# Kernel tuning notes

Measured on AMD Instinct MI355X. Metric: run time of the kernel, lower is better.

## Reference

```python
import jax, jax.numpy as jnp
import numpy as np

N, E = 50000, 1600000
IN_F, EDGE_F, HEADS, OUT_F = 64, 16, 4, 32
NEG_SLOPE = 0.2


def setup_inputs() -> dict:
    key = jax.random.key(0)
    ks = jax.random.split(key, 12)
    s = 0.05
    return {
        "x": jax.random.normal(ks[0], (N, IN_F), jnp.float32),
        "edge_index": jax.random.randint(ks[1], (2, E), 0, N, jnp.int32),
        "edge_attr": jax.random.normal(ks[2], (E, EDGE_F), jnp.float32),
        "W_lin": jax.random.normal(ks[3], (HEADS * OUT_F, IN_F), jnp.float32) * s,
        "w_s": jax.random.normal(ks[4], (OUT_F,), jnp.float32) * s,
        "b_s": jax.random.normal(ks[5], (), jnp.float32) * s,
        "w_t": jax.random.normal(ks[6], (OUT_F,), jnp.float32) * s,
        "b_t": jax.random.normal(ks[7], (), jnp.float32) * s,
        "W_edge": jax.random.normal(ks[8], (HEADS * OUT_F, EDGE_F), jnp.float32) * s,
        "w_e": jax.random.normal(ks[9], (OUT_F,), jnp.float32) * s,
        "b_e": jax.random.normal(ks[10], (), jnp.float32) * s,
        "W_res": jax.random.normal(ks[11], (HEADS * OUT_F, IN_F), jnp.float32) * s,
        "bias": jnp.zeros((HEADS * OUT_F,), jnp.float32),
    }


def reference(x, edge_index, edge_attr, W_lin, w_s, b_s, w_t, b_t, W_edge, w_e, b_e, W_res, bias):
    n = x.shape[0]
    src, dst = edge_index[0], edge_index[1]  # j = source, i = target

    # node projection: [N, H, F]
    xp = (x @ W_lin.T).reshape(n, HEADS, OUT_F)
    # attn_s/attn_t are Linear(F,1) then sum(-1) -> per-node per-head scalar
    a_s = xp @ w_s + b_s  # [N, H]
    a_t = xp @ w_t + b_t  # [N, H]

    # edge feature projection and attention term
    ep = (edge_attr @ W_edge.T).reshape(-1, HEADS, OUT_F)  # [E, H, F]
    a_e = ep @ w_e + b_e  # [E, H]

    # per-edge logits: alpha_j + alpha_i + alpha_edge, leaky_relu
    alpha = a_s[src] + a_t[dst] + a_e  # [E, H]
    alpha = jnp.where(alpha >= 0, alpha, NEG_SLOPE * alpha)

    # segment softmax over edges grouped by target node
    amax = jax.ops.segment_max(alpha, dst, num_segments=n)  # [N, H]
    expv = jnp.exp(alpha - amax[dst])  # [E, H]
    denom = jax.ops.segment_sum(expv, dst, num_segments=n)  # [N, H]
    attn = expv / denom[dst]  # [E, H]

    # weighted messages from source nodes, scatter-add to targets
    msg = attn[..., None] * xp[src]  # [E, H, F]
    out = jax.ops.segment_sum(msg, dst, num_segments=n)  # [N, H, F]
    out = out.reshape(n, HEADS * OUT_F)  # concat heads

    out = out + x @ W_res.T + bias
    return out
```

## Files before the change

kernel.cpp:

```cpp
#include <hip/hip_runtime.h>
#include <hip/hip_fp16.h>
#include <math.h>

#define HEADS 4
#define OUT_F 32
#define HF 128
#define IN_F 64
#define EDGE_F 16

typedef int   v4i __attribute__((ext_vector_type(4)));
typedef float v4f __attribute__((ext_vector_type(4)));
typedef float v2f __attribute__((ext_vector_type(2)));
typedef _Float16 v8h __attribute__((ext_vector_type(8)));


__global__ __launch_bounds__(256) void k_project_mfma(
    const float* __restrict__ x, const float* __restrict__ W_lin,
    const float* __restrict__ W_res, const float* __restrict__ bias,
    const float* __restrict__ w_s, const float* __restrict__ w_t,
    const float* __restrict__ b_s, const float* __restrict__ b_t,
    __half* __restrict__ xp, float* __restrict__ a_s, float* __restrict__ a_t,
    float* __restrict__ out, int* __restrict__ head, int N_, int PB) {
  if (blockIdx.x >= PB) {
    int i = (blockIdx.x - PB) * 256 + threadIdx.x;
    if (i < N_ * 4) head[i] = -1;
    return;
  }
  __shared__ __half sw[256][72];
  __shared__ __half sxh[64][72];
  int t = threadIdx.x;
  {
    const float* wsrc = (t < 128) ? (W_lin + t * IN_F) : (W_res + (size_t)(t - 128) * IN_F);
    const float4* w4 = (const float4*)wsrc;
#pragma unroll
    for (int k8 = 0; k8 < 8; k8++) {
      float4 f0 = w4[k8 * 2 + 0];
      float4 f1 = w4[k8 * 2 + 1];
      *(__half2*)(&sw[t][k8 * 8 + 0]) = __floats2half2_rn(f0.x, f0.y);
      *(__half2*)(&sw[t][k8 * 8 + 2]) = __floats2half2_rn(f0.z, f0.w);
      *(__half2*)(&sw[t][k8 * 8 + 4]) = __floats2half2_rn(f1.x, f1.y);
      *(__half2*)(&sw[t][k8 * 8 + 6]) = __floats2half2_rn(f1.z, f1.w);
    }
  }
  int n0 = blockIdx.x * 64;
  {
    int node = t >> 2, q = t & 3;
    int nn = n0 + node;
    const float4* xs = (const float4*)(x + (size_t)nn * IN_F) + q * 4;
#pragma unroll
    for (int j = 0; j < 4; j++) {
      float4 f = (nn < N_) ? xs[j] : make_float4(0.f, 0.f, 0.f, 0.f);
      int col = q * 16 + j * 4;
      *(__half2*)(&sxh[node][col + 0]) = __floats2half2_rn(f.x, f.y);
      *(__half2*)(&sxh[node][col + 2]) = __floats2half2_rn(f.z, f.w);
    }
  }
  __syncthreads();

  int w = t >> 6, l = t & 63;
  int lm = l & 15, lg = l >> 4;
  int mbase = n0 + w * 16;
  v8h a0 = *(const v8h*)(&sxh[w * 16 + lm][lg * 8]);
  v8h a1 = *(const v8h*)(&sxh[w * 16 + lm][32 + lg * 8]);

  float ws_lo = w_s[lm], ws_hi = w_s[16 + lm];
  float wt_lo = w_t[lm], wt_hi = w_t[16 + lm];
  float bsv = b_s[0], btv = b_t[0];

  float sacc[4] = {0.f, 0.f, 0.f, 0.f};
  float tacc[4] = {0.f, 0.f, 0.f, 0.f};

#pragma unroll
  for (int nt = 0; nt < 16; nt++) {
    v8h b0 = *(const v8h*)(&sw[nt * 16 + lm][lg * 8]);
    v8h b1 = *(const v8h*)(&sw[nt * 16 + lm][32 + lg * 8]);
    v4f d = {0.f, 0.f, 0.f, 0.f};
    d = __builtin_amdgcn_mfma_f32_16x16x32_f16(a0, b0, d, 0, 0, 0);
    d = __builtin_amdgcn_mfma_f32_16x16x32_f16(a1, b1, d, 0, 0, 0);
    if (nt < 8) {
      int c = nt * 16 + lm;
      float wssel = (nt & 1) ? ws_hi : ws_lo;
      float wtsel = (nt & 1) ? wt_hi : wt_lo;
#pragma unroll
      for (int reg = 0; reg < 4; reg++) {
        int m = mbase + lg * 4 + reg;
        if (m < N_) xp[(size_t)m * HF + c] = __float2half(d[reg]);
        sacc[reg] += d[reg] * wssel;
        tacc[reg] += d[reg] * wtsel;
      }
      if (nt & 1) {
        int h = nt >> 1;
#pragma unroll
        for (int reg = 0; reg < 4; reg++) {
#pragma unroll
          for (int dlt = 8; dlt > 0; dlt >>= 1) {
            sacc[reg] += __shfl_xor(sacc[reg], dlt, 64);
            tacc[reg] += __shfl_xor(tacc[reg], dlt, 64);
          }
        }
        if (lm == 0) {
#pragma unroll
          for (int reg = 0; reg < 4; reg++) {
            int m = mbase + lg * 4 + reg;
            if (m < N_) {
              a_s[m * 4 + h] = sacc[reg] + bsv;
              a_t[m * 4 + h] = tacc[reg] + btv;
            }
          }
        }
#pragma unroll
        for (int reg = 0; reg < 4; reg++) { sacc[reg] = 0.f; tacc[reg] = 0.f; }
      }
    } else {
      int c = (nt - 8) * 16 + lm;
      float bv = bias[c];
#pragma unroll
      for (int reg = 0; reg < 4; reg++) {
        int m = mbase + lg * 4 + reg;
        if (m < N_) out[(size_t)m * HF + c] = d[reg] + bv;
      }
    }
  }
}

__global__ __launch_bounds__(256) void k_edge_logits(
    const int* __restrict__ ei, const float* __restrict__ ea,
    const float* __restrict__ W_edge, const float* __restrict__ w_e,
    const float* __restrict__ b_e,
    const float* __restrict__ a_s, const float* __restrict__ a_t,
    int* __restrict__ head, v4i* __restrict__ pay, int E_) {
  __shared__ float sv[64];
  {
    int t = threadIdx.x;
    if (t < 64) {
      int h = t >> 4, cc = t & 15;
      float se = 0.f;
#pragma unroll
      for (int f = 0; f < 32; f++) se += W_edge[(h * 32 + f) * 16 + cc] * w_e[f];
      sv[t] = se;
    }
  }
  __syncthreads();
  int e = blockIdx.x * 256 + threadIdx.x;
  if (e >= E_) return;
  int src = ei[e], dst = ei[E_ + e];
  int nx = atomicExch(head + dst * 4 + (e & 3), e);
  float bev = b_e[0];
  const v4f* ea4 = (const v4f*)(ea + (size_t)e * EDGE_F);
  v4f e0 = __builtin_nontemporal_load(ea4 + 0);
  v4f e1 = __builtin_nontemporal_load(ea4 + 1);
  v4f e2 = __builtin_nontemporal_load(ea4 + 2);
  v4f e3 = __builtin_nontemporal_load(ea4 + 3);
  float4 as4 = *(const float4*)(a_s + src * 4);
  float4 at4 = *(const float4*)(a_t + dst * 4);
  float asv[4] = {as4.x, as4.y, as4.z, as4.w};
  float atv[4] = {at4.x, at4.y, at4.z, at4.w};
  float res[4];
#pragma unroll
  for (int h = 0; h < 4; h++) {
    const float* v = sv + h * 16;
    float ae =
        e0.x * v[0]  + e0.y * v[1]  + e0.z * v[2]  + e0.w * v[3]
      + e1.x * v[4]  + e1.y * v[5]  + e1.z * v[6]  + e1.w * v[7]
      + e2.x * v[8]  + e2.y * v[9]  + e2.z * v[10] + e2.w * v[11]
      + e3.x * v[12] + e3.y * v[13] + e3.z * v[14] + e3.w * v[15];
    float al = asv[h] + atv[h] + ae + bev;
    al = al >= 0.f ? al : 0.2f * al;
    res[h] = __expf(al);
  }
  __half2 h01 = __floats2half2_rn(res[0], res[1]);
  __half2 h23 = __floats2half2_rn(res[2], res[3]);
  v4i pk;
  pk.x = src;
  pk.y = *(int*)&h01;
  pk.z = *(int*)&h23;
  pk.w = nx;
  pay[e] = pk;
}

__global__ __launch_bounds__(256) void k_gather(
    const int* __restrict__ head, const v4i* __restrict__ pay,
    const __half* __restrict__ xp, float* __restrict__ out, int N_, int E_) {
  int wid = threadIdx.x >> 6, lane = threadIdx.x & 63;
  int n = blockIdx.x * 4 + wid;
  if (n >= N_) return;
  int e0 = head[n * 4 + 0], e1 = head[n * 4 + 1];
  int e2 = head[n * 4 + 2], e3 = head[n * 4 + 3];
  if ((e0 & e1 & e2 & e3) < 0 && e0 < 0 && e1 < 0 && e2 < 0 && e3 < 0)
    return;
  int h = lane >> 4;
  float2 acc = make_float2(0.f, 0.f);
  float se = 0.f;
#define EXTRACT_EV(P, EV)                                                \
  {                                                                      \
    unsigned hw = (h < 2) ? (unsigned)(P).y : (unsigned)(P).z;           \
    unsigned bits = (h & 1) ? (hw >> 16) : (hw & 0xffffu);               \
    EV = __half2float(__ushort_as_half((unsigned short)bits));           \
  }
#define ROW_FMA(P, EV)                                                   \
  {                                                                      \
    const __half2* xr = (const __half2*)(xp + (size_t)(P).x * HF);       \
    float2 xv = __half22float2(xr[lane]);                                \
    acc.x += (EV) * xv.x;                                                \
    acc.y += (EV) * xv.y;                                                \
    se += (EV);                                                          \
  }
  while ((e0 | e1 | e2 | e3) >= 0) {
    v4i p0 = pay[e0];
    v4i p1 = pay[e1];
    v4i p2 = pay[e2];
    v4i p3 = pay[e3];
    float ev0, ev1, ev2, ev3;
    EXTRACT_EV(p0, ev0);
    EXTRACT_EV(p1, ev1);
    EXTRACT_EV(p2, ev2);
    EXTRACT_EV(p3, ev3);
    ROW_FMA(p0, ev0);
    ROW_FMA(p1, ev1);
    ROW_FMA(p2, ev2);
    ROW_FMA(p3, ev3);
    e0 = p0.w;
    e1 = p1.w;
    e2 = p2.w;
    e3 = p3.w;
  }
  for (int it = 0; it < E_; ++it) {
    if (e0 < 0 && e1 < 0 && e2 < 0 && e3 < 0) break;
    int s0 = e0 < 0 ? 0 : e0, s1 = e1 < 0 ? 0 : e1;
    int s2 = e2 < 0 ? 0 : e2, s3 = e3 < 0 ? 0 : e3;
    v4i p0 = pay[s0];
    v4i p1 = pay[s1];
    v4i p2 = pay[s2];
    v4i p3 = pay[s3];
    float m0 = e0 < 0 ? 0.f : 1.f, m1 = e1 < 0 ? 0.f : 1.f;
    float m2 = e2 < 0 ? 0.f : 1.f, m3 = e3 < 0 ? 0.f : 1.f;
    float ev0, ev1, ev2, ev3;
    EXTRACT_EV(p0, ev0);
    EXTRACT_EV(p1, ev1);
    EXTRACT_EV(p2, ev2);
    EXTRACT_EV(p3, ev3);
    ev0 *= m0; ev1 *= m1; ev2 *= m2; ev3 *= m3;
    ROW_FMA(p0, ev0);
    ROW_FMA(p1, ev1);
    ROW_FMA(p2, ev2);
    ROW_FMA(p3, ev3);
    e0 = e0 < 0 ? e0 : p0.w;
    e1 = e1 < 0 ? e1 : p1.w;
    e2 = e2 < 0 ? e2 : p2.w;
    e3 = e3 < 0 ? e3 : p3.w;
  }
#undef EXTRACT_EV
#undef ROW_FMA
  float r = 1.f / se;
  size_t oi = (size_t)n * 64 + lane;
  v2f o = __builtin_nontemporal_load((const v2f*)out + oi);
  o.x += acc.x * r;
  o.y += acc.y * r;
  __builtin_nontemporal_store(o, (v2f*)out + oi);
}

extern "C" void kernel_launch(void* const* d_in, const int* in_sizes, int n_in,
                              void* d_out, int out_size, void* d_ws, size_t ws_size,
                              hipStream_t stream) {
  const float* x      = (const float*)d_in[0];
  const int*   ei     = (const int*)  d_in[1];
  const float* ea     = (const float*)d_in[2];
  const float* W_lin  = (const float*)d_in[3];
  const float* w_s    = (const float*)d_in[4];
  const float* b_s    = (const float*)d_in[5];
  const float* w_t    = (const float*)d_in[6];
  const float* b_t    = (const float*)d_in[7];
  const float* W_edge = (const float*)d_in[8];
  const float* w_e    = (const float*)d_in[9];
  const float* b_e    = (const float*)d_in[10];
  const float* W_res  = (const float*)d_in[11];
  const float* bias   = (const float*)d_in[12];
  int N_ = in_sizes[0] / IN_F;
  int E_ = in_sizes[1] / 2;
  float* out = (float*)d_out;

  __half* xp    = (__half*)d_ws;
  v4i*    pay   = (v4i*)(xp + (size_t)N_ * HF);
  float*  a_s   = (float*)(pay + E_);
  float*  a_t   = a_s + (size_t)N_ * 4;
  int*    head  = (int*)(a_t + (size_t)N_ * 4);

  int PB = (N_ + 63) / 64;
  int HB = (N_ * 4 + 255) / 256;

  k_project_mfma<<<PB + HB, 256, 0, stream>>>(
      x, W_lin, W_res, bias, w_s, w_t, b_s, b_t, xp, a_s, a_t, out, head, N_, PB);
  k_edge_logits<<<(E_ + 255) / 256, 256, 0, stream>>>(
      ei, ea, W_edge, w_e, b_e, a_s, a_t, head, pay, E_);
  k_gather<<<(N_ + 3) / 4, 256, 0, stream>>>(head, pay, xp, out, N_, E_);
}
```

Measured before the change: 362.1 us.

## Use eight per-block-striped linked-list heads per node and walk eight chains

Changes the per-node edge linked lists from four interleaved heads (chosen by edge index) to eight stripe-major head arrays chosen by block index. This is meant to spread the atomicExch traffic and give the gather kernel eight independent pointer chains, so more dependent loads are in flight per wave. The gather loop is merged into a single masked loop covering all eight chains. The cost is twice as much head initialization, eight head loads per node, and masked dummy loads once chains become uneven, which happens more often with about 32 edges split across eight chains.

```diff
diff --git a/kernel.cpp b/kernel.cpp
--- a/kernel.cpp
+++ b/kernel.cpp
@@ -23,7 +23,7 @@
     float* __restrict__ out, int* __restrict__ head, int N_, int PB) {
   if (blockIdx.x >= PB) {
     int i = (blockIdx.x - PB) * 256 + threadIdx.x;
-    if (i < N_ * 4) head[i] = -1;
+    if (i < N_ * 8) head[i] = -1;
     return;
   }
   __shared__ __half sw[256][72];
@@ -128,7 +128,7 @@
     const float* __restrict__ W_edge, const float* __restrict__ w_e,
     const float* __restrict__ b_e,
     const float* __restrict__ a_s, const float* __restrict__ a_t,
-    int* __restrict__ head, v4i* __restrict__ pay, int E_) {
+    int* __restrict__ head, v4i* __restrict__ pay, int N_, int E_) {
   __shared__ float sv[64];
   {
     int t = threadIdx.x;
@@ -144,7 +144,8 @@
   int e = blockIdx.x * 256 + threadIdx.x;
   if (e >= E_) return;
   int src = ei[e], dst = ei[E_ + e];
-  int nx = atomicExch(head + dst * 4 + (e & 3), e);
+  int stripe = blockIdx.x & 7;
+  int nx = atomicExch(head + stripe * N_ + dst, e);
   float bev = b_e[0];
   const v4f* ea4 = (const v4f*)(ea + (size_t)e * EDGE_F);
   v4f e0 = __builtin_nontemporal_load(ea4 + 0);
@@ -184,18 +185,22 @@
   int wid = threadIdx.x >> 6, lane = threadIdx.x & 63;
   int n = blockIdx.x * 4 + wid;
   if (n >= N_) return;
-  int e0 = head[n * 4 + 0], e1 = head[n * 4 + 1];
-  int e2 = head[n * 4 + 2], e3 = head[n * 4 + 3];
-  if ((e0 & e1 & e2 & e3) < 0 && e0 < 0 && e1 < 0 && e2 < 0 && e3 < 0)
+  int e0 = head[0 * N_ + n], e1 = head[1 * N_ + n];
+  int e2 = head[2 * N_ + n], e3 = head[3 * N_ + n];
+  int e4 = head[4 * N_ + n], e5 = head[5 * N_ + n];
+  int e6 = head[6 * N_ + n], e7 = head[7 * N_ + n];
+  if ((e0 & e1 & e2 & e3 & e4 & e5 & e6 & e7) < 0 &&
+      e0 < 0 && e1 < 0 && e2 < 0 && e3 < 0 &&
+      e4 < 0 && e5 < 0 && e6 < 0 && e7 < 0)
     return;
   int h = lane >> 4;
   float2 acc = make_float2(0.f, 0.f);
   float se = 0.f;
-#define EXTRACT_EV(P, EV)                                                \
+#define EV_OF(P, M, EV)                                                  \
   {                                                                      \
     unsigned hw = (h < 2) ? (unsigned)(P).y : (unsigned)(P).z;           \
     unsigned bits = (h & 1) ? (hw >> 16) : (hw & 0xffffu);               \
-    EV = __half2float(__ushort_as_half((unsigned short)bits));           \
+    EV = (M) * __half2float(__ushort_as_half((unsigned short)bits));     \
   }
 #define ROW_FMA(P, EV)                                                   \
   {                                                                      \
@@ -205,51 +210,51 @@
     acc.y += (EV) * xv.y;                                                \
     se += (EV);                                                          \
   }
-  while ((e0 | e1 | e2 | e3) >= 0) {
-    v4i p0 = pay[e0];
-    v4i p1 = pay[e1];
-    v4i p2 = pay[e2];
-    v4i p3 = pay[e3];
-    float ev0, ev1, ev2, ev3;
-    EXTRACT_EV(p0, ev0);
-    EXTRACT_EV(p1, ev1);
-    EXTRACT_EV(p2, ev2);
-    EXTRACT_EV(p3, ev3);
+  for (int it = 0; it < E_; ++it) {
+    if ((e0 & e1 & e2 & e3 & e4 & e5 & e6 & e7) < 0) break;
+    int s0 = e0 < 0 ? 0 : e0, s1 = e1 < 0 ? 0 : e1;
+    int s2 = e2 < 0 ? 0 : e2, s3 = e3 < 0 ? 0 : e3;
+    int s4 = e4 < 0 ? 0 : e4, s5 = e5 < 0 ? 0 : e5;
+    int s6 = e6 < 0 ? 0 : e6, s7 = e7 < 0 ? 0 : e7;
+    v4i p0 = pay[s0];
+    v4i p1 = pay[s1];
+    v4i p2 = pay[s2];
+    v4i p3 = pay[s3];
+    v4i p4 = pay[s4];
+    v4i p5 = pay[s5];
+    v4i p6 = pay[s6];
+    v4i p7 = pay[s7];
+    float m0 = e0 < 0 ? 0.f : 1.f, m1 = e1 < 0 ? 0.f : 1.f;
+    float m2 = e2 < 0 ? 0.f : 1.f, m3 = e3 < 0 ? 0.f : 1.f;
+    float m4 = e4 < 0 ? 0.f : 1.f, m5 = e5 < 0 ? 0.f : 1.f;
+    float m6 = e6 < 0 ? 0.f : 1.f, m7 = e7 < 0 ? 0.f : 1.f;
+    float ev0, ev1, ev2, ev3, ev4, ev5, ev6, ev7;
+    EV_OF(p0, m0, ev0);
+    EV_OF(p1, m1, ev1);
+    EV_OF(p2, m2, ev2);
+    EV_OF(p3, m3, ev3);
+    EV_OF(p4, m4, ev4);
+    EV_OF(p5, m5, ev5);
+    EV_OF(p6, m6, ev6);
+    EV_OF(p7, m7, ev7);
     ROW_FMA(p0, ev0);
     ROW_FMA(p1, ev1);
     ROW_FMA(p2, ev2);
     ROW_FMA(p3, ev3);
-    e0 = p0.w;
-    e1 = p1.w;
-    e2 = p2.w;
-    e3 = p3.w;
-  }
-  for (int it = 0; it < E_; ++it) {
-    if (e0 < 0 && e1 < 0 && e2 < 0 && e3 < 0) break;
-    int s0 = e0 < 0 ? 0 : e0, s1 = e1 < 0 ? 0 : e1;
-    int s2 = e2 < 0 ? 0 : e2, s3 = e3 < 0 ? 0 : e3;
-    v4i p0 = pay[s0];
-    v4i p1 = pay[s1];
-    v4i p2 = pay[s2];
-    v4i p3 = pay[s3];
-    float m0 = e0 < 0 ? 0.f : 1.f, m1 = e1 < 0 ? 0.f : 1.f;
-    float m2 = e2 < 0 ? 0.f : 1.f, m3 = e3 < 0 ? 0.f : 1.f;
-    float ev0, ev1, ev2, ev3;
-    EXTRACT_EV(p0, ev0);
-    EXTRACT_EV(p1, ev1);
-    EXTRACT_EV(p2, ev2);
-    EXTRACT_EV(p3, ev3);
-    ev0 *= m0; ev1 *= m1; ev2 *= m2; ev3 *= m3;
-    ROW_FMA(p0, ev0);
-    ROW_FMA(p1, ev1);
-    ROW_FMA(p2, ev2);
-    ROW_FMA(p3, ev3);
+    ROW_FMA(p4, ev4);
+    ROW_FMA(p5, ev5);
+    ROW_FMA(p6, ev6);
+    ROW_FMA(p7, ev7);
     e0 = e0 < 0 ? e0 : p0.w;
     e1 = e1 < 0 ? e1 : p1.w;
     e2 = e2 < 0 ? e2 : p2.w;
     e3 = e3 < 0 ? e3 : p3.w;
-  }
-#undef EXTRACT_EV
+    e4 = e4 < 0 ? e4 : p4.w;
+    e5 = e5 < 0 ? e5 : p5.w;
+    e6 = e6 < 0 ? e6 : p6.w;
+    e7 = e7 < 0 ? e7 : p7.w;
+  }
+#undef EV_OF
 #undef ROW_FMA
   float r = 1.f / se;
   size_t oi = (size_t)n * 64 + lane;
@@ -286,11 +291,11 @@
   int*    head  = (int*)(a_t + (size_t)N_ * 4);
 
   int PB = (N_ + 63) / 64;
-  int HB = (N_ * 4 + 255) / 256;
+  int HB = (N_ * 8 + 255) / 256;
 
   k_project_mfma<<<PB + HB, 256, 0, stream>>>(
       x, W_lin, W_res, bias, w_s, w_t, b_s, b_t, xp, a_s, a_t, out, head, N_, PB);
   k_edge_logits<<<(E_ + 255) / 256, 256, 0, stream>>>(
-      ei, ea, W_edge, w_e, b_e, a_s, a_t, head, pay, E_);
+      ei, ea, W_edge, w_e, b_e, a_s, a_t, head, pay, N_, E_);
   k_gather<<<(N_ + 3) / 4, 256, 0, stream>>>(head, pay, xp, out, N_, E_);
 }
```

Result: slower. 376.9 us (+4.1%).
